# Optimization experiments

Measured on AMD Instinct MI355X. Metric: run time of the kernel, lower is better.

Reference implementation:

```python
import jax, jax.numpy as jnp
import numpy as np

IN_FEATURES = 4096
OUT_FEATURES = 11008
N_TOKENS = 8192


def setup_inputs() -> dict:
    key = jax.random.key(0)
    kx, kw, kb = jax.random.split(key, 3)
    x = jax.random.normal(kx, (N_TOKENS, IN_FEATURES), dtype=jnp.float32)
    # nn.Linear weight: [out_features, in_features]
    bound = 1.0 / np.sqrt(IN_FEATURES)
    weight = jax.random.uniform(kw, (OUT_FEATURES, IN_FEATURES), dtype=jnp.float32,
                                minval=-bound, maxval=bound)
    bias = jax.random.uniform(kb, (OUT_FEATURES,), dtype=jnp.float32,
                              minval=-bound, maxval=bound)
    return {"x": x, "weight": weight, "bias": bias}


def reference(x, weight, bias):
    # Ternarize weights to {-1, 0, +1} then standard dense matmul + bias.
    ternary_w = jnp.sign(weight)  # [out, in]
    return jnp.matmul(x, ternary_w.T) + bias  # [n_tokens, out]
```

## Files before the change

kernel.cpp:

```cpp
#include <hip/hip_runtime.h>
#include <stdint.h>

#define M_DIM 8192
#define N_DIM 11008
#define K_DIM 4096

#define BM 256
#define BN 256
#define BK 64
#define NT (K_DIM / BK)
#define GRID_M (M_DIM / BM)
#define GRID_N (N_DIM / BN)
#define NWG (GRID_M * GRID_N)

#define BUFB (BM * BK)

typedef int i32x4 __attribute__((ext_vector_type(4)));

__device__ __forceinline__ void gload16(const int8_t* src, int8_t* dst) {
    __builtin_amdgcn_global_load_lds(
        (const __attribute__((address_space(1))) uint32_t*)src,
        (__attribute__((address_space(3))) uint32_t*)dst, 16, 0, 0);
}


__global__ __launch_bounds__(256) void quant_x_kernel(
    const float* __restrict__ x, int8_t* __restrict__ xq, float* __restrict__ sinv)
{
    const int wave = blockIdx.x * 4 + (threadIdx.x >> 6);
    const int lane = threadIdx.x & 63;
    const float* row = x + (size_t)wave * K_DIM;

    float4 v[16];
    float mx = 0.0f;
    #pragma unroll
    for (int j = 0; j < 16; ++j) {
        v[j] = *(const float4*)(row + (j * 64 + lane) * 4);
        mx = fmaxf(mx, fmaxf(fmaxf(fabsf(v[j].x), fabsf(v[j].y)),
                             fmaxf(fabsf(v[j].z), fabsf(v[j].w))));
    }
    #pragma unroll
    for (int off = 32; off > 0; off >>= 1)
        mx = fmaxf(mx, __shfl_xor(mx, off));
    if (mx < 1e-30f) mx = 1e-30f;
    const float s = 127.0f / mx;

    int8_t* orow = xq + (size_t)wave * K_DIM;
    #pragma unroll
    for (int j = 0; j < 16; ++j) {
        int a = (int)__builtin_rintf(v[j].x * s);
        int b = (int)__builtin_rintf(v[j].y * s);
        int c = (int)__builtin_rintf(v[j].z * s);
        int d = (int)__builtin_rintf(v[j].w * s);
        uint32_t p = (uint32_t)(a & 0xFF) | ((uint32_t)(b & 0xFF) << 8) |
                     ((uint32_t)(c & 0xFF) << 16) | ((uint32_t)(d & 0xFF) << 24);
        *(uint32_t*)(orow + (j * 64 + lane) * 4) = p;
    }
    if (lane == 0) sinv[wave] = mx / 127.0f;
}


__global__ __launch_bounds__(256) void sign_w_kernel(
    const float* __restrict__ w, int8_t* __restrict__ wq, long long n16)
{
    long long i = (long long)blockIdx.x * blockDim.x + threadIdx.x;
    const long long stride = (long long)gridDim.x * blockDim.x;
    for (; i < n16; i += stride) {
        const float* src = w + i * 16;
        uint32_t pk[4];
        #pragma unroll
        for (int q = 0; q < 4; ++q) {
            float4 f = *(const float4*)(src + q * 4);
            int a = (f.x > 0.f) ? 1 : ((f.x < 0.f) ? -1 : 0);
            int b = (f.y > 0.f) ? 1 : ((f.y < 0.f) ? -1 : 0);
            int c = (f.z > 0.f) ? 1 : ((f.z < 0.f) ? -1 : 0);
            int d = (f.w > 0.f) ? 1 : ((f.w < 0.f) ? -1 : 0);
            pk[q] = (uint32_t)(a & 0xFF) | ((uint32_t)(b & 0xFF) << 8) |
                    ((uint32_t)(c & 0xFF) << 16) | ((uint32_t)(d & 0xFF) << 24);
        }
        *(i32x4*)(wq + i * 16) = (i32x4){(int)pk[0], (int)pk[1], (int)pk[2], (int)pk[3]};
    }
}


__global__ __launch_bounds__(512, 2) void ternary_gemm_i8(
    const int8_t* __restrict__ A, const int8_t* __restrict__ B,
    const float* __restrict__ bias, const float* __restrict__ sinv,
    float* __restrict__ out)
{
    extern __shared__ int8_t lds[];
    int8_t* As = lds;
    int8_t* Bs = lds + 3 * BUFB;

    const int tid  = threadIdx.x;
    const int lane = tid & 63;
    const int wid  = tid >> 6;
    const int wm   = wid >> 2;
    const int wn   = wid & 3;
    const int l15  = lane & 15;
    const int l4   = lane >> 4;

    const int bid = blockIdx.x;
    const int swz = (bid & 7) * (NWG / 8) + (bid >> 3);
    const int bm  = swz / GRID_N;
    const int bn  = swz % GRID_N;
    const long brow = (long)bm * BM;
    const long bcol = (long)bn * BN;

    const int rowt = tid >> 2;
    const int ssrc = (tid & 3) ^ ((tid >> 3) & 3);
    const int8_t* pA = A + (size_t)(brow + rowt) * K_DIM + ssrc * 16;
    const int8_t* pB = B + (size_t)(bcol + rowt) * K_DIM + ssrc * 16;

    auto stageAB = [&](int t, int bslot) {
        #pragma unroll
        for (int r = 0; r < 2; ++r)
            gload16(pA + (size_t)r * 128 * K_DIM + (size_t)t * BK,
                    As + bslot * BUFB + r * 8192 + wid * 1024);
        #pragma unroll
        for (int r = 0; r < 2; ++r)
            gload16(pB + (size_t)r * 128 * K_DIM + (size_t)t * BK,
                    Bs + bslot * BUFB + r * 8192 + wid * 1024);
    };

    const int slot = l4 ^ ((l15 >> 1) & 3);
    const int aOff = (wm * 16 + l15) * 64 + slot * 16;
    const int bOff = (wn * 16 + l15) * 64 + slot * 16;

    i32x4 acc[8][4];
    #pragma unroll
    for (int m = 0; m < 8; ++m)
        #pragma unroll
        for (int n = 0; n < 4; ++n) acc[m][n] = (i32x4){0, 0, 0, 0};

    stageAB(0, 0);
    stageAB(1, 1);
    stageAB(2, 2);
    asm volatile("s_waitcnt vmcnt(8)" ::: "memory");
    __builtin_amdgcn_s_barrier();
    __builtin_amdgcn_sched_barrier(0);

    int bcur = 0;
    for (int t = 0; t < NT; ++t) {
        const int b = bcur;

        i32x4 ar[8], br[4];
        #pragma unroll
        for (int m = 0; m < 8; ++m)
            ar[m] = *(const i32x4*)(As + b * BUFB + m * 2048 + aOff);
        #pragma unroll
        for (int n = 0; n < 4; ++n)
            br[n] = *(const i32x4*)(Bs + b * BUFB + n * 4096 + bOff);
        __builtin_amdgcn_sched_barrier(0);
        asm volatile("s_waitcnt lgkmcnt(0)" ::: "memory");
        __builtin_amdgcn_s_barrier();
        __builtin_amdgcn_sched_barrier(0);

        if (t + 3 < NT) stageAB(t + 3, b);
        __builtin_amdgcn_sched_barrier(0);

        __builtin_amdgcn_s_setprio(1);
        #pragma unroll
        for (int m = 0; m < 8; ++m)
            #pragma unroll
            for (int n = 0; n < 4; ++n)
                acc[m][n] = __builtin_amdgcn_mfma_i32_16x16x64_i8(ar[m], br[n], acc[m][n], 0, 0, 0);
        __builtin_amdgcn_s_setprio(0);
        __builtin_amdgcn_sched_barrier(0);

        if (t <= NT - 4)      { asm volatile("s_waitcnt vmcnt(8)" ::: "memory"); }
        else if (t == NT - 3) { asm volatile("s_waitcnt vmcnt(4)" ::: "memory"); }
        else                  { asm volatile("s_waitcnt vmcnt(0)" ::: "memory"); }
        __builtin_amdgcn_s_barrier();
        __builtin_amdgcn_sched_barrier(0);

        bcur = (bcur == 2) ? 0 : bcur + 1;
    }

    int   cols[4];
    float bv[4];
    #pragma unroll
    for (int n = 0; n < 4; ++n) {
        cols[n] = (int)bcol + n * 64 + wn * 16 + l15;
        bv[n] = bias[cols[n]];
    }
    #pragma unroll
    for (int m = 0; m < 8; ++m) {
        const size_t row0 = (size_t)brow + m * 32 + wm * 16 + l4 * 4;
        float s0 = sinv[row0], s1 = sinv[row0 + 1], s2 = sinv[row0 + 2], s3 = sinv[row0 + 3];
        #pragma unroll
        for (int n = 0; n < 4; ++n) {
            out[(row0 + 0) * N_DIM + cols[n]] = (float)acc[m][n][0] * s0 + bv[n];
            out[(row0 + 1) * N_DIM + cols[n]] = (float)acc[m][n][1] * s1 + bv[n];
            out[(row0 + 2) * N_DIM + cols[n]] = (float)acc[m][n][2] * s2 + bv[n];
            out[(row0 + 3) * N_DIM + cols[n]] = (float)acc[m][n][3] * s3 + bv[n];
        }
    }
}


__global__ void naive_kernel(const float* __restrict__ x, const float* __restrict__ w,
                             const float* __restrict__ bias, float* __restrict__ out) {
    long long o = (long long)blockIdx.x * blockDim.x + threadIdx.x;
    if (o >= (long long)M_DIM * N_DIM) return;
    int row = (int)(o / N_DIM), col = (int)(o % N_DIM);
    float s = 0.0f;
    const float* xr = x + (size_t)row * K_DIM;
    const float* wr = w + (size_t)col * K_DIM;
    for (int k = 0; k < K_DIM; ++k) {
        float wv = wr[k];
        s += (wv > 0.0f) ? xr[k] : ((wv < 0.0f) ? -xr[k] : 0.0f);
    }
    out[o] = s + bias[col];
}


extern "C" void kernel_launch(void* const* d_in, const int* in_sizes, int n_in,
                              void* d_out, int out_size, void* d_ws, size_t ws_size,
                              hipStream_t stream) {
    const float* x    = (const float*)d_in[0];
    const float* w    = (const float*)d_in[1];
    const float* bias = (const float*)d_in[2];
    float* out        = (float*)d_out;

    const size_t xq_bytes = (size_t)M_DIM * K_DIM;
    const size_t wq_bytes = (size_t)N_DIM * K_DIM;
    const size_t si_bytes = (size_t)M_DIM * sizeof(float);

    if (ws_size >= xq_bytes + wq_bytes + si_bytes) {
        int8_t* xq   = (int8_t*)d_ws;
        int8_t* wq   = (int8_t*)((char*)d_ws + xq_bytes);
        float*  sinv = (float*)((char*)d_ws + xq_bytes + wq_bytes);

        quant_x_kernel<<<M_DIM / 4, 256, 0, stream>>>(x, xq, sinv);
        const long long n16 = ((long long)N_DIM * K_DIM) / 16;
        sign_w_kernel<<<2048, 256, 0, stream>>>(w, wq, n16);

        hipFuncSetAttribute(reinterpret_cast<const void*>(ternary_gemm_i8),
                            hipFuncAttributeMaxDynamicSharedMemorySize, 6 * BUFB);
        ternary_gemm_i8<<<NWG, 512, 6 * BUFB, stream>>>(xq, wq, bias, sinv, out);
    } else {
        const long long total = (long long)M_DIM * N_DIM;
        naive_kernel<<<(int)((total + 255) / 256), 256, 0, stream>>>(x, w, bias, out);
    }
}
```

Baseline: 497.3 us.

## Deepen LDS ring to five stages and double-buffer MFMA fragments in registers

```diff
diff --git a/kernel.cpp b/kernel.cpp
--- a/kernel.cpp
+++ b/kernel.cpp
@@ -13,7 +13,8 @@
 #define GRID_N (N_DIM / BN)
 #define NWG (GRID_M * GRID_N)
 
-#define BUFB (BM * BK)
+#define BUF (BM * BK)
+#define NRING 5
 
 typedef int i32x4 __attribute__((ext_vector_type(4)));
 
@@ -90,7 +91,7 @@
 {
     extern __shared__ int8_t lds[];
     int8_t* As = lds;
-    int8_t* Bs = lds + 3 * BUFB;
+    int8_t* Bs = lds + NRING * BUF;
 
     const int tid  = threadIdx.x;
     const int lane = tid & 63;
@@ -116,11 +117,11 @@
         #pragma unroll
         for (int r = 0; r < 2; ++r)
             gload16(pA + (size_t)r * 128 * K_DIM + (size_t)t * BK,
-                    As + bslot * BUFB + r * 8192 + wid * 1024);
+                    As + bslot * BUF + r * 8192 + wid * 1024 + (lane << 4));
         #pragma unroll
         for (int r = 0; r < 2; ++r)
             gload16(pB + (size_t)r * 128 * K_DIM + (size_t)t * BK,
-                    Bs + bslot * BUFB + r * 8192 + wid * 1024);
+                    Bs + bslot * BUF + r * 8192 + wid * 1024 + (lane << 4));
     };
 
     const int slot = l4 ^ ((l15 >> 1) & 3);
@@ -133,30 +134,37 @@
         #pragma unroll
         for (int n = 0; n < 4; ++n) acc[m][n] = (i32x4){0, 0, 0, 0};
 
-    stageAB(0, 0);
-    stageAB(1, 1);
-    stageAB(2, 2);
+    i32x4 arA[8], brA[4], arB[8], brB[4];
+
+    auto readFrags = [&](int t, i32x4 (&ar)[8], i32x4 (&br)[4]) {
+        const int s = t % NRING;
+        const int8_t* Ab = As + s * BUF;
+        const int8_t* Bb = Bs + s * BUF;
+        #pragma unroll
+        for (int m = 0; m < 8; ++m) ar[m] = *(const i32x4*)(Ab + m * 2048 + aOff);
+        #pragma unroll
+        for (int n = 0; n < 4; ++n) br[n] = *(const i32x4*)(Bb + n * 4096 + bOff);
+    };
+
+    stageAB(0, 0); stageAB(1, 1); stageAB(2, 2); stageAB(3, 3);
     asm volatile("s_waitcnt vmcnt(8)" ::: "memory");
     __builtin_amdgcn_s_barrier();
     __builtin_amdgcn_sched_barrier(0);
-
-    int bcur = 0;
-    for (int t = 0; t < NT; ++t) {
-        const int b = bcur;
-
-        i32x4 ar[8], br[4];
-        #pragma unroll
-        for (int m = 0; m < 8; ++m)
-            ar[m] = *(const i32x4*)(As + b * BUFB + m * 2048 + aOff);
-        #pragma unroll
-        for (int n = 0; n < 4; ++n)
-            br[n] = *(const i32x4*)(Bs + b * BUFB + n * 4096 + bOff);
-        __builtin_amdgcn_sched_barrier(0);
-        asm volatile("s_waitcnt lgkmcnt(0)" ::: "memory");
-        __builtin_amdgcn_s_barrier();
-        __builtin_amdgcn_sched_barrier(0);
-
-        if (t + 3 < NT) stageAB(t + 3, b);
+    readFrags(0, arA, brA);
+    __builtin_amdgcn_sched_barrier(0);
+
+    auto body = [&](int t, i32x4 (&arc)[8], i32x4 (&brc)[4],
+                           i32x4 (&arn)[8], i32x4 (&brn)[4]) {
+        if (t + 1 < NT) {
+            readFrags(t + 1, arn, brn);
+            __builtin_amdgcn_sched_barrier(0);
+            asm volatile("s_waitcnt lgkmcnt(12)" ::: "memory");
+        } else {
+            asm volatile("s_waitcnt lgkmcnt(0)" ::: "memory");
+        }
+        __builtin_amdgcn_sched_barrier(0);
+
+        if (t + 4 < NT) stageAB(t + 4, (t + 4) % NRING);
         __builtin_amdgcn_sched_barrier(0);
 
         __builtin_amdgcn_s_setprio(1);
@@ -164,17 +172,20 @@
         for (int m = 0; m < 8; ++m)
             #pragma unroll
             for (int n = 0; n < 4; ++n)
-                acc[m][n] = __builtin_amdgcn_mfma_i32_16x16x64_i8(ar[m], br[n], acc[m][n], 0, 0, 0);
+                acc[m][n] = __builtin_amdgcn_mfma_i32_16x16x64_i8(arc[m], brc[n], acc[m][n], 0, 0, 0);
         __builtin_amdgcn_s_setprio(0);
         __builtin_amdgcn_sched_barrier(0);
 
-        if (t <= NT - 4)      { asm volatile("s_waitcnt vmcnt(8)" ::: "memory"); }
-        else if (t == NT - 3) { asm volatile("s_waitcnt vmcnt(4)" ::: "memory"); }
+        if (t <= NT - 5)      { asm volatile("s_waitcnt vmcnt(8)" ::: "memory"); }
+        else if (t == NT - 4) { asm volatile("s_waitcnt vmcnt(4)" ::: "memory"); }
         else                  { asm volatile("s_waitcnt vmcnt(0)" ::: "memory"); }
         __builtin_amdgcn_s_barrier();
         __builtin_amdgcn_sched_barrier(0);
-
-        bcur = (bcur == 2) ? 0 : bcur + 1;
+    };
+
+    for (int t = 0; t < NT; t += 2) {
+        body(t,     arA, brA, arB, brB);
+        body(t + 1, arB, brB, arA, brA);
     }
 
     int   cols[4];
@@ -236,9 +247,10 @@
         const long long n16 = ((long long)N_DIM * K_DIM) / 16;
         sign_w_kernel<<<2048, 256, 0, stream>>>(w, wq, n16);
 
+        const int lds_bytes = NRING * 2 * BUF;
         hipFuncSetAttribute(reinterpret_cast<const void*>(ternary_gemm_i8),
-                            hipFuncAttributeMaxDynamicSharedMemorySize, 6 * BUFB);
-        ternary_gemm_i8<<<NWG, 512, 6 * BUFB, stream>>>(xq, wq, bias, sinv, out);
+                            hipFuncAttributeMaxDynamicSharedMemorySize, lds_bytes);
+        ternary_gemm_i8<<<NWG, 512, lds_bytes, stream>>>(xq, wq, bias, sinv, out);
     } else {
         const long long total = (long long)M_DIM * N_DIM;
         naive_kernel<<<(int)((total + 255) / 256), 256, 0, stream>>>(x, w, bias, out);
```

Result: faster. 481.9 us (-3.1%).

## Use 16-wave blocks with 64x64 wave tiles and a four-slot LDS ring

Applied to the files above, without the earlier changes.

```diff
diff --git a/kernel.cpp b/kernel.cpp
--- a/kernel.cpp
+++ b/kernel.cpp
@@ -13,7 +13,8 @@
 #define GRID_N (N_DIM / BN)
 #define NWG (GRID_M * GRID_N)
 
-#define BUFB (BM * BK)
+#define BUF (BM * BK)
+#define NRING 4
 
 typedef int i32x4 __attribute__((ext_vector_type(4)));
 
@@ -83,20 +84,20 @@
 }
 
 
-__global__ __launch_bounds__(512, 2) void ternary_gemm_i8(
+__global__ __launch_bounds__(1024, 4) void ternary_gemm_i8(
     const int8_t* __restrict__ A, const int8_t* __restrict__ B,
     const float* __restrict__ bias, const float* __restrict__ sinv,
     float* __restrict__ out)
 {
     extern __shared__ int8_t lds[];
     int8_t* As = lds;
-    int8_t* Bs = lds + 3 * BUFB;
+    int8_t* Bs = lds + NRING * BUF;
 
     const int tid  = threadIdx.x;
     const int lane = tid & 63;
     const int wid  = tid >> 6;
-    const int wm   = wid >> 2;
-    const int wn   = wid & 3;
+    const int wr   = wid >> 2;
+    const int wc   = wid & 3;
     const int l15  = lane & 15;
     const int l4   = lane >> 4;
 
@@ -113,80 +114,64 @@
     const int8_t* pB = B + (size_t)(bcol + rowt) * K_DIM + ssrc * 16;
 
     auto stageAB = [&](int t, int bslot) {
-        #pragma unroll
-        for (int r = 0; r < 2; ++r)
-            gload16(pA + (size_t)r * 128 * K_DIM + (size_t)t * BK,
-                    As + bslot * BUFB + r * 8192 + wid * 1024);
-        #pragma unroll
-        for (int r = 0; r < 2; ++r)
-            gload16(pB + (size_t)r * 128 * K_DIM + (size_t)t * BK,
-                    Bs + bslot * BUFB + r * 8192 + wid * 1024);
+        gload16(pA + (size_t)t * BK, As + bslot * BUF + tid * 16);
+        gload16(pB + (size_t)t * BK, Bs + bslot * BUF + tid * 16);
     };
 
     const int slot = l4 ^ ((l15 >> 1) & 3);
-    const int aOff = (wm * 16 + l15) * 64 + slot * 16;
-    const int bOff = (wn * 16 + l15) * 64 + slot * 16;
-
-    i32x4 acc[8][4];
-    #pragma unroll
-    for (int m = 0; m < 8; ++m)
+    const int aOff = (wr * 64 + l15) * 64 + slot * 16;
+    const int bOff = (wc * 64 + l15) * 64 + slot * 16;
+
+    i32x4 acc[4][4];
+    #pragma unroll
+    for (int m = 0; m < 4; ++m)
         #pragma unroll
         for (int n = 0; n < 4; ++n) acc[m][n] = (i32x4){0, 0, 0, 0};
 
-    stageAB(0, 0);
-    stageAB(1, 1);
-    stageAB(2, 2);
-    asm volatile("s_waitcnt vmcnt(8)" ::: "memory");
+    stageAB(0, 0); stageAB(1, 1); stageAB(2, 2);
+    asm volatile("s_waitcnt vmcnt(4)" ::: "memory");
     __builtin_amdgcn_s_barrier();
     __builtin_amdgcn_sched_barrier(0);
 
-    int bcur = 0;
     for (int t = 0; t < NT; ++t) {
-        const int b = bcur;
-
-        i32x4 ar[8], br[4];
-        #pragma unroll
-        for (int m = 0; m < 8; ++m)
-            ar[m] = *(const i32x4*)(As + b * BUFB + m * 2048 + aOff);
+        const int b = t & 3;
+
+        i32x4 ar[4], br[4];
+        #pragma unroll
+        for (int m = 0; m < 4; ++m)
+            ar[m] = *(const i32x4*)(As + b * BUF + m * 1024 + aOff);
         #pragma unroll
         for (int n = 0; n < 4; ++n)
-            br[n] = *(const i32x4*)(Bs + b * BUFB + n * 4096 + bOff);
-        __builtin_amdgcn_sched_barrier(0);
-        asm volatile("s_waitcnt lgkmcnt(0)" ::: "memory");
-        __builtin_amdgcn_s_barrier();
-        __builtin_amdgcn_sched_barrier(0);
-
-        if (t + 3 < NT) stageAB(t + 3, b);
-        __builtin_amdgcn_sched_barrier(0);
+            br[n] = *(const i32x4*)(Bs + b * BUF + n * 1024 + bOff);
+
+        if (t + 3 < NT) stageAB(t + 3, (t + 3) & 3);
 
         __builtin_amdgcn_s_setprio(1);
         #pragma unroll
-        for (int m = 0; m < 8; ++m)
+        for (int m = 0; m < 4; ++m)
             #pragma unroll
             for (int n = 0; n < 4; ++n)
                 acc[m][n] = __builtin_amdgcn_mfma_i32_16x16x64_i8(ar[m], br[n], acc[m][n], 0, 0, 0);
         __builtin_amdgcn_s_setprio(0);
         __builtin_amdgcn_sched_barrier(0);
 
-        if (t <= NT - 4)      { asm volatile("s_waitcnt vmcnt(8)" ::: "memory"); }
-        else if (t == NT - 3) { asm volatile("s_waitcnt vmcnt(4)" ::: "memory"); }
+        if (t <= NT - 4)      { asm volatile("s_waitcnt vmcnt(4)" ::: "memory"); }
+        else if (t == NT - 3) { asm volatile("s_waitcnt vmcnt(2)" ::: "memory"); }
         else                  { asm volatile("s_waitcnt vmcnt(0)" ::: "memory"); }
         __builtin_amdgcn_s_barrier();
         __builtin_amdgcn_sched_barrier(0);
-
-        bcur = (bcur == 2) ? 0 : bcur + 1;
     }
 
     int   cols[4];
     float bv[4];
     #pragma unroll
     for (int n = 0; n < 4; ++n) {
-        cols[n] = (int)bcol + n * 64 + wn * 16 + l15;
+        cols[n] = (int)bcol + wc * 64 + n * 16 + l15;
         bv[n] = bias[cols[n]];
     }
     #pragma unroll
-    for (int m = 0; m < 8; ++m) {
-        const size_t row0 = (size_t)brow + m * 32 + wm * 16 + l4 * 4;
+    for (int m = 0; m < 4; ++m) {
+        const size_t row0 = (size_t)brow + wr * 64 + m * 16 + l4 * 4;
         float s0 = sinv[row0], s1 = sinv[row0 + 1], s2 = sinv[row0 + 2], s3 = sinv[row0 + 3];
         #pragma unroll
         for (int n = 0; n < 4; ++n) {
@@ -236,9 +221,10 @@
         const long long n16 = ((long long)N_DIM * K_DIM) / 16;
         sign_w_kernel<<<2048, 256, 0, stream>>>(w, wq, n16);
 
+        const int lds_bytes = NRING * 2 * BUF;
         hipFuncSetAttribute(reinterpret_cast<const void*>(ternary_gemm_i8),
-                            hipFuncAttributeMaxDynamicSharedMemorySize, 6 * BUFB);
-        ternary_gemm_i8<<<NWG, 512, 6 * BUFB, stream>>>(xq, wq, bias, sinv, out);
+                            hipFuncAttributeMaxDynamicSharedMemorySize, lds_bytes);
+        ternary_gemm_i8<<<NWG, 1024, lds_bytes, stream>>>(xq, wq, bias, sinv, out);
     } else {
         const long long total = (long long)M_DIM * N_DIM;
         naive_kernel<<<(int)((total + 255) / 256), 256, 0, stream>>>(x, w, bias, out);
```

Result: faster. 463.8 us (-6.7%).
